# Performance work log

Measured on AMD Instinct MI355X. Metric: run time of the kernel, lower is better.

The kernel has to match this reference:

```python
import jax, jax.numpy as jnp
import numpy as np

N_HEAD_FULL = 16  # config.n_head

def setup_inputs() -> dict:
    key = jax.random.key(0)
    ks = jax.random.split(key, 5)
    B, T, D = 2, 2048, 2048
    s = 0.02
    return {
        "x": jax.random.normal(ks[0], (B, T, D), dtype=jnp.float32),
        "Wq": jax.random.normal(ks[1], (D, D), dtype=jnp.float32) * s,
        "Wk": jax.random.normal(ks[2], (D, D), dtype=jnp.float32) * s,
        "Wv": jax.random.normal(ks[3], (D, D), dtype=jnp.float32) * s,
        "Wo": jax.random.normal(ks[4], (D, D), dtype=jnp.float32) * s,
        "active_dim": 1024,
        "active_kv": 64,
    }

def reference(x, Wq, Wk, Wv, Wo, active_dim, active_kv):
    B, T, D = x.shape
    d = active_dim if active_dim is not None else D
    head_dim_base = D // N_HEAD_FULL          # 128
    kv_dim = active_kv if active_kv is not None else head_dim_base
    n_head = d // head_dim_base               # active heads
    head_dim = d // n_head                    # == head_dim_base

    xs = x[..., :d]                            # [B,T,d]
    # F.linear(x, W[:d,:d]) == x @ W[:d,:d].T
    q = jnp.einsum('btc,dc->btd', xs, Wq[:d, :d])
    k = jnp.einsum('btc,dc->btd', xs, Wk[:d, :d])
    v = jnp.einsum('btc,dc->btd', xs, Wv[:d, :d])

    def split_heads(t):  # [B,T,d] -> [B,h,T,hd]
        return t.reshape(B, T, n_head, head_dim).transpose(0, 2, 1, 3)
    q, k, v = split_heads(q), split_heads(k), split_heads(v)

    if kv_dim < head_dim:
        q, k, v = q[..., :kv_dim], k[..., :kv_dim], v[..., :kv_dim]

    scale = 1.0 / np.sqrt(kv_dim).astype(np.float32)
    attn = jnp.einsum('bhqd,bhkd->bhqk', q, k) * scale  # [B,h,T,T]
    causal = jnp.tril(jnp.ones((T, T), dtype=bool))
    attn = jnp.where(causal, attn, jnp.float32(-jnp.inf))
    attn = jax.nn.softmax(attn, axis=-1)
    out = jnp.einsum('bhqk,bhkd->bhqd', attn, v)        # [B,h,T,kv]

    if kv_dim < head_dim:
        out = jnp.pad(out, ((0, 0), (0, 0), (0, 0), (0, head_dim - kv_dim)))
    out = out.transpose(0, 2, 1, 3).reshape(B, T, d)
    out = jnp.einsum('btc,dc->btd', out, Wo[:d, :d])
    if d < D:
        out = jnp.pad(out, ((0, 0), (0, 0), (0, D - d)))
    return out
```

## Files before the change

### kernel.cpp

```cpp
#include <hip/hip_runtime.h>
#include <hip/hip_bf16.h>

typedef __attribute__((ext_vector_type(8))) short bf16x8;
typedef __attribute__((ext_vector_type(4))) float f32x4;

#define MFMA16(a,b,c) __builtin_amdgcn_mfma_f32_16x16x32_bf16((a),(b),(c),0,0,0)

static __device__ __forceinline__ unsigned short f2bf(float f) {
    unsigned int u = __builtin_bit_cast(unsigned int, f);
    u += 0x7fffu + ((u >> 16) & 1u);
    return (unsigned short)(u >> 16);
}

static __device__ __forceinline__ void g2l16(const unsigned short* g, unsigned short* l) {
    __builtin_amdgcn_global_load_lds(
        (const __attribute__((address_space(1))) unsigned int*)g,
        (__attribute__((address_space(3))) unsigned int*)l,
        16, 0, 0);
}

#define BT     4096
#define DFULL  2048
#define DACT   1024
#define DKV    64
#define NSEL   512
#define TSEQ   2048
#define PADR   72

__global__ __launch_bounds__(256) void prep_kernel(
    const float* __restrict__ x,  const float* __restrict__ Wq,
    const float* __restrict__ Wk, const float* __restrict__ Wv,
    const float* __restrict__ Wo,
    unsigned short* __restrict__ xb,  unsigned short* __restrict__ Wqb,
    unsigned short* __restrict__ Wkb, unsigned short* __restrict__ Wvb,
    unsigned short* __restrict__ Wob, float* __restrict__ out)
{
    const int NA = (BT * DACT) / 8;
    const int NB = (NSEL * DACT) / 8;
    const int NC = (DACT * NSEL) / 8;
    const int ND = (BT * DACT) / 8;
    const int TOT = NA + 3 * NB + NC + ND;
    for (int u = blockIdx.x * blockDim.x + threadIdx.x; u < TOT;
         u += gridDim.x * blockDim.x) {
        if (u < NA) {
            int e = u * 8; int row = e >> 10, col = e & 1023;
            const float* s = x + (size_t)row * DFULL + col;
            f32x4 v0 = *(const f32x4*)s, v1 = *(const f32x4*)(s + 4);
            bf16x8 o;
            #pragma unroll
            for (int j = 0; j < 4; ++j) { o[j] = (short)f2bf(v0[j]); o[4+j] = (short)f2bf(v1[j]); }
            *(bf16x8*)(xb + e) = o;
        } else if (u < NA + 3 * NB) {
            int t = u - NA; int mat = t / NB; int q = t % NB;
            int e = q * 8; int n = e >> 10, c = e & 1023;
            const float* W = (mat == 0) ? Wq : (mat == 1) ? Wk : Wv;
            unsigned short* Wb = (mat == 0) ? Wqb : (mat == 1) ? Wkb : Wvb;
            int wrow = (n >> 6) * 128 + (n & 63);
            const float* s = W + (size_t)wrow * DFULL + c;
            f32x4 v0 = *(const f32x4*)s, v1 = *(const f32x4*)(s + 4);
            bf16x8 o;
            #pragma unroll
            for (int j = 0; j < 4; ++j) { o[j] = (short)f2bf(v0[j]); o[4+j] = (short)f2bf(v1[j]); }
            *(bf16x8*)(Wb + e) = o;
        } else if (u < NA + 3 * NB + NC) {
            int q = u - NA - 3 * NB;
            int e = q * 8; int r = e >> 9, cs = e & 511;
            int col = (cs >> 6) * 128 + (cs & 63);
            const float* s = Wo + (size_t)r * DFULL + col;
            f32x4 v0 = *(const f32x4*)s, v1 = *(const f32x4*)(s + 4);
            bf16x8 o;
            #pragma unroll
            for (int j = 0; j < 4; ++j) { o[j] = (short)f2bf(v0[j]); o[4+j] = (short)f2bf(v1[j]); }
            *(bf16x8*)(Wob + e) = o;
        } else {
            int q = u - (NA + 3 * NB + NC);
            int e = q * 8; int row = e >> 10, col = e & 1023;
            float* dp = out + (size_t)row * DFULL + DACT + col;
            f32x4 z = {0.f, 0.f, 0.f, 0.f};
            *(f32x4*)dp = z; *(f32x4*)(dp + 4) = z;
        }
    }
}

__global__ __launch_bounds__(256) void qkv_gemm(
    const unsigned short* __restrict__ xb,
    const unsigned short* __restrict__ Wall,
    unsigned short* __restrict__ Qb, unsigned short* __restrict__ Kb,
    unsigned short* __restrict__ Vb)
{
    __shared__ unsigned short As[64 * 64];
    __shared__ unsigned short Bs[128 * 64];
    const int m0 = blockIdx.x * 64, n0 = blockIdx.y * 128;
    const int tid = threadIdx.x, w = tid >> 6, l = tid & 63;
    const int lr = l & 15, g = l >> 4, lk = g * 8;
    const int wr = w >> 1, wc = w & 1;
    const int srow = l >> 3, scol = (l & 7) * 8;

    f32x4 acc[2][4] = {};
    for (int k0 = 0; k0 < DACT; k0 += 64) {
        __syncthreads();
        #pragma unroll
        for (int i = 0; i < 2; ++i) {
            int chunk = w * 2 + i;
            int row = chunk * 8 + srow;
            g2l16(&xb[(size_t)(m0 + row) * DACT + k0 + scol], &As[chunk * 512]);
        }
        #pragma unroll
        for (int i = 0; i < 4; ++i) {
            int chunk = w * 4 + i;
            int row = chunk * 8 + srow;
            g2l16(&Wall[(size_t)(n0 + row) * DACT + k0 + scol], &Bs[chunk * 512]);
        }
        __syncthreads();
        #pragma unroll
        for (int kk = 0; kk < 64; kk += 32) {
            bf16x8 a[2], b[4];
            #pragma unroll
            for (int m = 0; m < 2; ++m)
                a[m] = *(const bf16x8*)&As[(wr * 32 + m * 16 + lr) * 64 + kk + lk];
            #pragma unroll
            for (int n = 0; n < 4; ++n)
                b[n] = *(const bf16x8*)&Bs[(wc * 64 + n * 16 + lr) * 64 + kk + lk];
            #pragma unroll
            for (int m = 0; m < 2; ++m)
                #pragma unroll
                for (int n = 0; n < 4; ++n)
                    acc[m][n] = MFMA16(a[m], b[n], acc[m][n]);
        }
    }
    #pragma unroll
    for (int m = 0; m < 2; ++m)
        #pragma unroll
        for (int n = 0; n < 4; ++n)
            #pragma unroll
            for (int i = 0; i < 4; ++i) {
                int row = m0 + wr * 32 + m * 16 + g * 4 + i;
                int col = n0 + wc * 64 + n * 16 + lr;
                int mat = col >> 9, r = col & 511, h = r >> 6, j = r & 63;
                int bb = row >> 11, t = row & 2047, bh = bb * 8 + h;
                float v = acc[m][n][i];
                if (mat == 0)
                    Qb[((size_t)bh * TSEQ + t) * DKV + j] = f2bf(v * 0.125f);
                else if (mat == 1)
                    Kb[((size_t)bh * TSEQ + t) * DKV + (j ^ ((t & 7) << 3))] = f2bf(v);
                else
                    Vb[((size_t)bh * TSEQ + t) * DKV + j] = f2bf(v);
            }
}

__global__ __launch_bounds__(256) void vtrans_kernel(
    const unsigned short* __restrict__ Vb, unsigned short* __restrict__ Vtb)
{
    __shared__ unsigned short Ls[64 * PADR];
    const int t0 = blockIdx.x * 64, bh = blockIdx.y;
    const int tid = threadIdx.x;
    #pragma unroll
    for (int it = 0; it < 2; ++it) {
        int r = (tid >> 3) + it * 32, c = (tid & 7) * 8;
        *(bf16x8*)&Ls[r * PADR + c] =
            *(const bf16x8*)&Vb[((size_t)bh * TSEQ + t0 + r) * DKV + c];
    }
    __syncthreads();
    int dv = tid >> 2, tt0 = (tid & 3) * 16;
    unsigned short tmp[16];
    #pragma unroll
    for (int j = 0; j < 16; ++j) tmp[j] = Ls[(tt0 + j) * PADR + dv];
    const int sw = (dv & 7) << 3;
    size_t tb = (((size_t)bh * 32 + (t0 >> 6)) * 64 + dv) * 64;
    *(bf16x8*)&Vtb[tb + (tt0 ^ sw)]       = *(bf16x8*)&tmp[0];
    *(bf16x8*)&Vtb[tb + ((tt0 + 8) ^ sw)] = *(bf16x8*)&tmp[8];
}

__global__ __launch_bounds__(512, 4) void attn_kernel(
    const unsigned short* __restrict__ Qb,
    const unsigned short* __restrict__ Kb,
    const unsigned short* __restrict__ Vtb,
    unsigned short* __restrict__ att)
{
    __shared__ unsigned short KV[2][2][2][4096];
    __shared__ unsigned short Ps[8][16 * 64];
    const int f = blockIdx.x;
    const int bh = f & 15;
    const int S = 31 - (f >> 4);
    const int ntt = S + 1;
    const int np = (ntt + 1) >> 1;
    const int tid = threadIdx.x, w = tid >> 6, l = tid & 63;
    const int lr = l & 15, g = l >> 4, lk = g * 8;
    const int s = w >> 1, j = w & 1;
    const size_t kvb = (size_t)bh * TSEQ * DKV;
    const int bb = bh >> 3, h = bh & 7;
    const int qs0 = S * 64 + s * 16;

    unsigned short* Psw = Ps[w];
    const short os = (short)0x3F80;
    const bf16x8 ones = {os, os, os, os, os, os, os, os};

    bf16x8 qf0 = *(const bf16x8*)&Qb[kvb + (size_t)(qs0 + lr) * DKV + lk];
    bf16x8 qf1 = *(const bf16x8*)&Qb[kvb + (size_t)(qs0 + lr) * DKV + 32 + lk];

    f32x4 acc[4] = {};
    f32x4 dacc = {};

    #define STAGE(b, p)                                                        \
        do {                                                                   \
            int r_ = w >> 1, par_ = r_ >> 1, kv_ = r_ & 1;                     \
            int t_ = 2 * (p) + par_;                                           \
            if (t_ < ntt) {                                                    \
                const unsigned short* src_ =                                   \
                    (kv_ ? Vtb : Kb) + kvb + (size_t)t_ * 4096 + (w & 1) * 2048; \
                unsigned short* dst_ = &KV[b][par_][kv_][(w & 1) * 2048];      \
                g2l16(&src_[l * 8],        dst_);                              \
                g2l16(&src_[512 + l * 8],  dst_ + 512);                        \
                g2l16(&src_[1024 + l * 8], dst_ + 1024);                       \
                g2l16(&src_[1536 + l * 8], dst_ + 1536);                       \
            }                                                                  \
        } while (0)

    STAGE(0, 0);
    __syncthreads();

    for (int p = 0; p < np; ++p) {
        const int cur = p & 1;
        if (p + 1 < np) STAGE(cur ^ 1, p + 1);

        const int jt = 2 * p + j;
        if (jt < ntt) {
            const unsigned short* Kt = KV[cur][j][0];
            const unsigned short* Vt = KV[cur][j][1];

            #pragma unroll
            for (int c = 0; c < 4; ++c) {
                const int row = c * 16 + lr, sr = (row & 7) << 3;
                bf16x8 b0 = *(const bf16x8*)&Kt[row * 64 + (lk ^ sr)];
                bf16x8 b1 = *(const bf16x8*)&Kt[row * 64 + ((32 + lk) ^ sr)];
                f32x4 z = {};
                z = MFMA16(qf0, b0, z);
                z = MFMA16(qf1, b1, z);
                if (jt == ntt - 1) {
                    int kcol = jt * 64 + c * 16 + lr;
                    #pragma unroll
                    for (int i = 0; i < 4; ++i)
                        if (kcol > qs0 + g * 4 + i) z[i] = -64.f;
                }
                #pragma unroll
                for (int i = 0; i < 4; ++i) {
                    const int prow = g * 4 + i;
                    Psw[prow * 64 + ((c * 16 + lr) ^ ((prow & 7) << 3))] =
                        f2bf(__expf(z[i]));
                }
            }
            const int psr = (lr & 7) << 3;
            bf16x8 pa0 = *(const bf16x8*)&Psw[lr * 64 + (lk ^ psr)];
            bf16x8 pa1 = *(const bf16x8*)&Psw[lr * 64 + ((32 + lk) ^ psr)];

            #pragma unroll
            for (int n = 0; n < 4; ++n) {
                const int row = n * 16 + lr, sr = (row & 7) << 3;
                bf16x8 v0 = *(const bf16x8*)&Vt[row * 64 + (lk ^ sr)];
                bf16x8 v1 = *(const bf16x8*)&Vt[row * 64 + ((32 + lk) ^ sr)];
                acc[n] = MFMA16(pa0, v0, acc[n]);
                acc[n] = MFMA16(pa1, v1, acc[n]);
            }
            dacc = MFMA16(pa0, ones, dacc);
            dacc = MFMA16(pa1, ones, dacc);
        }
        __syncthreads();
    }
    #undef STAGE

    float* M = (float*)KV;
    if (j == 1) {
        #pragma unroll
        for (int n = 0; n < 4; ++n)
            #pragma unroll
            for (int i = 0; i < 4; ++i)
                M[s * 1088 + (g * 4 + i) * 64 + n * 16 + lr] = acc[n][i];
        if (lr == 0) {
            #pragma unroll
            for (int i = 0; i < 4; ++i)
                M[s * 1088 + 1024 + g * 4 + i] = dacc[i];
        }
    }
    __syncthreads();
    if (j == 0) {
        #pragma unroll
        for (int i = 0; i < 4; ++i) {
            float den = dacc[i] + M[s * 1088 + 1024 + g * 4 + i];
            float inv = 1.0f / den;
            int t = qs0 + g * 4 + i;
            #pragma unroll
            for (int n = 0; n < 4; ++n) {
                float v = acc[n][i] + M[s * 1088 + (g * 4 + i) * 64 + n * 16 + lr];
                att[((size_t)bb * TSEQ + t) * NSEL + h * 64 + n * 16 + lr] =
                    f2bf(v * inv);
            }
        }
    }
}

__global__ __launch_bounds__(256) void oproj_gemm(
    const unsigned short* __restrict__ att,
    const unsigned short* __restrict__ Wob,
    float* __restrict__ out)
{
    __shared__ unsigned short As[128 * 64];
    __shared__ unsigned short Bs[128 * 64];
    const int m0 = blockIdx.x * 128, n0 = blockIdx.y * 128;
    const int tid = threadIdx.x, w = tid >> 6, l = tid & 63;
    const int lr = l & 15, g = l >> 4, lk = g * 8;
    const int wr = w >> 1, wc = w & 1;
    const int srow = l >> 3, scol = (l & 7) * 8;

    f32x4 acc[4][4] = {};
    for (int k0 = 0; k0 < NSEL; k0 += 64) {
        __syncthreads();
        #pragma unroll
        for (int i = 0; i < 4; ++i) {
            int chunk = w * 4 + i;
            int row = chunk * 8 + srow;
            g2l16(&att[(size_t)(m0 + row) * NSEL + k0 + scol], &As[chunk * 512]);
            g2l16(&Wob[(size_t)(n0 + row) * NSEL + k0 + scol], &Bs[chunk * 512]);
        }
        __syncthreads();
        #pragma unroll
        for (int kk = 0; kk < 64; kk += 32) {
            bf16x8 a[4], b[4];
            #pragma unroll
            for (int m = 0; m < 4; ++m)
                a[m] = *(const bf16x8*)&As[(wr * 64 + m * 16 + lr) * 64 + kk + lk];
            #pragma unroll
            for (int n = 0; n < 4; ++n)
                b[n] = *(const bf16x8*)&Bs[(wc * 64 + n * 16 + lr) * 64 + kk + lk];
            #pragma unroll
            for (int m = 0; m < 4; ++m)
                #pragma unroll
                for (int n = 0; n < 4; ++n)
                    acc[m][n] = MFMA16(a[m], b[n], acc[m][n]);
        }
    }
    #pragma unroll
    for (int m = 0; m < 4; ++m)
        #pragma unroll
        for (int n = 0; n < 4; ++n)
            #pragma unroll
            for (int i = 0; i < 4; ++i) {
                int row = m0 + wr * 64 + m * 16 + g * 4 + i;
                int col = n0 + wc * 64 + n * 16 + lr;
                out[(size_t)row * DFULL + col] = acc[m][n][i];
            }
}

extern "C" void kernel_launch(void* const* d_in, const int* in_sizes, int n_in,
                              void* d_out, int out_size, void* d_ws, size_t ws_size,
                              hipStream_t stream) {
    const float* x  = (const float*)d_in[0];
    const float* Wq = (const float*)d_in[1];
    const float* Wk = (const float*)d_in[2];
    const float* Wv = (const float*)d_in[3];
    const float* Wo = (const float*)d_in[4];
    float* out = (float*)d_out;

    char* ws = (char*)d_ws;
    unsigned short* xb  = (unsigned short*)(ws);
    unsigned short* Wqb = (unsigned short*)(ws + 8388608);
    unsigned short* Wkb = (unsigned short*)(ws + 9437184);
    unsigned short* Wvb = (unsigned short*)(ws + 10485760);
    unsigned short* Wob = (unsigned short*)(ws + 11534336);
    unsigned short* Qb  = (unsigned short*)(ws + 12582912);
    unsigned short* Kb  = (unsigned short*)(ws + 16777216);
    unsigned short* Vtb = (unsigned short*)(ws + 20971520);
    unsigned short* Vb  = (unsigned short*)(ws + 25165824);
    unsigned short* att = (unsigned short*)(ws + 25165824);

    prep_kernel<<<2048, 256, 0, stream>>>(x, Wq, Wk, Wv, Wo,
                                          xb, Wqb, Wkb, Wvb, Wob, out);
    qkv_gemm<<<dim3(64, 12), 256, 0, stream>>>(xb, Wqb, Qb, Kb, Vb);
    vtrans_kernel<<<dim3(32, 16), 256, 0, stream>>>(Vb, Vtb);
    attn_kernel<<<512, 512, 0, stream>>>(Qb, Kb, Vtb, att);
    oproj_gemm<<<dim3(32, 8), 256, 0, stream>>>(att, Wob, out);
}
```

Before: 83.58 us.

## Move zero-padding into oproj grid, swap GEMM grid axes, rebalance causal attention order

The zero-fill of the unused output half moves out of the prep kernel into extra blocks of the output-projection GEMM. Those blocks sit alongside the compute blocks, so the fill overlaps GEMM work instead of lengthening the serial prep pass. Both GEMMs swap grid axes so consecutive blocks share the same A rows, which should improve L2 reuse. The attention kernel's second half of blocks now processes query tiles in ascending rather than descending order, mixing long and short causal tiles to balance the tail.

```diff
diff --git a/kernel.cpp b/kernel.cpp
--- a/kernel.cpp
+++ b/kernel.cpp
@@ -33,13 +33,12 @@
     const float* __restrict__ Wo,
     unsigned short* __restrict__ xb,  unsigned short* __restrict__ Wqb,
     unsigned short* __restrict__ Wkb, unsigned short* __restrict__ Wvb,
-    unsigned short* __restrict__ Wob, float* __restrict__ out)
+    unsigned short* __restrict__ Wob)
 {
     const int NA = (BT * DACT) / 8;
     const int NB = (NSEL * DACT) / 8;
     const int NC = (DACT * NSEL) / 8;
-    const int ND = (BT * DACT) / 8;
-    const int TOT = NA + 3 * NB + NC + ND;
+    const int TOT = NA + 3 * NB + NC;
     for (int u = blockIdx.x * blockDim.x + threadIdx.x; u < TOT;
          u += gridDim.x * blockDim.x) {
         if (u < NA) {
@@ -62,7 +61,7 @@
             #pragma unroll
             for (int j = 0; j < 4; ++j) { o[j] = (short)f2bf(v0[j]); o[4+j] = (short)f2bf(v1[j]); }
             *(bf16x8*)(Wb + e) = o;
-        } else if (u < NA + 3 * NB + NC) {
+        } else {
             int q = u - NA - 3 * NB;
             int e = q * 8; int r = e >> 9, cs = e & 511;
             int col = (cs >> 6) * 128 + (cs & 63);
@@ -72,12 +71,6 @@
             #pragma unroll
             for (int j = 0; j < 4; ++j) { o[j] = (short)f2bf(v0[j]); o[4+j] = (short)f2bf(v1[j]); }
             *(bf16x8*)(Wob + e) = o;
-        } else {
-            int q = u - (NA + 3 * NB + NC);
-            int e = q * 8; int row = e >> 10, col = e & 1023;
-            float* dp = out + (size_t)row * DFULL + DACT + col;
-            f32x4 z = {0.f, 0.f, 0.f, 0.f};
-            *(f32x4*)dp = z; *(f32x4*)(dp + 4) = z;
         }
     }
 }
@@ -90,7 +83,7 @@
 {
     __shared__ unsigned short As[64 * 64];
     __shared__ unsigned short Bs[128 * 64];
-    const int m0 = blockIdx.x * 64, n0 = blockIdx.y * 128;
+    const int m0 = blockIdx.y * 64, n0 = blockIdx.x * 128;
     const int tid = threadIdx.x, w = tid >> 6, l = tid & 63;
     const int lr = l & 15, g = l >> 4, lk = g * 8;
     const int wr = w >> 1, wc = w & 1;
@@ -180,8 +173,8 @@
     __shared__ unsigned short KV[2][2][2][4096];
     __shared__ unsigned short Ps[8][16 * 64];
     const int f = blockIdx.x;
-    const int bh = f & 15;
-    const int S = 31 - (f >> 4);
+    const int k = f & 255, bh = k & 15, pi = k >> 4;
+    const int S = (f < 256) ? (31 - pi) : pi;
     const int ntt = S + 1;
     const int np = (ntt + 1) >> 1;
     const int tid = threadIdx.x, w = tid >> 6, l = tid & 63;
@@ -303,10 +296,23 @@
     const unsigned short* __restrict__ Wob,
     float* __restrict__ out)
 {
+    const int tid = threadIdx.x;
+    if (blockIdx.x >= 8) {
+        const int m0z = blockIdx.y * 128;
+        const int n0z = DACT + (blockIdx.x - 8) * 128;
+        const f32x4 z = {0.f, 0.f, 0.f, 0.f};
+        #pragma unroll
+        for (int i = 0; i < 16; ++i) {
+            int chunk = tid + i * 256;
+            int row = chunk >> 5, c = (chunk & 31) * 4;
+            *(f32x4*)&out[(size_t)(m0z + row) * DFULL + n0z + c] = z;
+        }
+        return;
+    }
     __shared__ unsigned short As[128 * 64];
     __shared__ unsigned short Bs[128 * 64];
-    const int m0 = blockIdx.x * 128, n0 = blockIdx.y * 128;
-    const int tid = threadIdx.x, w = tid >> 6, l = tid & 63;
+    const int m0 = blockIdx.y * 128, n0 = blockIdx.x * 128;
+    const int w = tid >> 6, l = tid & 63;
     const int lr = l & 15, g = l >> 4, lk = g * 8;
     const int wr = w >> 1, wc = w & 1;
     const int srow = l >> 3, scol = (l & 7) * 8;
@@ -373,9 +379,9 @@
     unsigned short* att = (unsigned short*)(ws + 25165824);
 
     prep_kernel<<<2048, 256, 0, stream>>>(x, Wq, Wk, Wv, Wo,
-                                          xb, Wqb, Wkb, Wvb, Wob, out);
-    qkv_gemm<<<dim3(64, 12), 256, 0, stream>>>(xb, Wqb, Qb, Kb, Vb);
+                                          xb, Wqb, Wkb, Wvb, Wob);
+    qkv_gemm<<<dim3(12, 64), 256, 0, stream>>>(xb, Wqb, Qb, Kb, Vb);
     vtrans_kernel<<<dim3(32, 16), 256, 0, stream>>>(Vb, Vtb);
     attn_kernel<<<512, 512, 0, stream>>>(Qb, Kb, Vtb, att);
-    oproj_gemm<<<dim3(32, 8), 256, 0, stream>>>(att, Wob, out);
-}
+    oproj_gemm<<<dim3(16, 32), 256, 0, stream>>>(att, Wob, out);
+}
```

Result: slower. 85.57 us (+2.4%).
